# Optimization experiments

Measured on AMD Instinct MI355X. Metric: run time of the kernel, lower is better.

## Reference

```python
import jax, jax.numpy as jnp
import numpy as np

B, F, D = 4096, 64, 256  # batch, feature fields, embedding dim


def setup_inputs() -> dict:
    key = jax.random.key(0)
    inputs = jax.random.normal(key, (B, F, D), dtype=jnp.float32)
    return {"inputs": inputs}


def reference(inputs) -> jnp.ndarray:
    # Batched Gram matrix over the field axis: [B, F, F]
    gram = jnp.einsum('bid,bjd->bij', inputs, inputs)
    # Strict upper triangle (i < j), matching matrix_band_part(0,-1) - band_part(0,0)
    f = inputs.shape[1]
    iu, ju = jnp.triu_indices(f, k=1)
    # Gather the F*(F-1)/2 pairwise interactions per batch row -> [B, P]
    return gram[:, iu, ju]
```

## Files before the change

kernel.cpp:

```cpp
#include <hip/hip_runtime.h>

#define BATCH 4096
#define FF 64
#define DD 256
#define PAD 264
#define NPAIR 2016

typedef __attribute__((ext_vector_type(8))) short short8;
typedef __attribute__((ext_vector_type(16))) float f32x16;

__device__ __forceinline__ unsigned short f2bf(float f) {
    unsigned int u = __float_as_uint(f);
    u += 0x7FFFu + ((u >> 16) & 1u);
    return (unsigned short)(u >> 16);
}

__global__ __launch_bounds__(256, 4) void gram_tri(const float* __restrict__ x,
                                                   float* __restrict__ out) {
    __shared__ __align__(16) unsigned short sX[FF * PAD];
    const int b = blockIdx.x;
    const int t = threadIdx.x;

    const float4* __restrict__ src = (const float4*)(x + (size_t)b * (FF * DD));
#pragma unroll
    for (int it = 0; it < 16; ++it) {
        int idx = (it << 8) + t;
        float4 v = src[idx];
        int r  = idx >> 6;
        int kq = idx & 63;
        ushort4 w;
        w.x = f2bf(v.x); w.y = f2bf(v.y); w.z = f2bf(v.z); w.w = f2bf(v.w);
        *(ushort4*)&sX[r * PAD + (kq << 2)] = w;
    }
    __syncthreads();

    const int wave = t >> 6;
    const int lane = t & 63;
    const int qi = wave >> 1;
    const int qj = wave & 1;
    const int rA = (qi << 5) + (lane & 31);
    const int rB = (qj << 5) + (lane & 31);
    const int ks = (lane >> 5) << 3;

    f32x16 acc;
#pragma unroll
    for (int i = 0; i < 16; ++i) acc[i] = 0.0f;

    const unsigned short* pA = &sX[rA * PAD + ks];
    const unsigned short* pB = &sX[rB * PAD + ks];
#pragma unroll
    for (int ko = 0; ko < DD; ko += 16) {
        short8 a  = *(const short8*)(pA + ko);
        short8 bb = *(const short8*)(pB + ko);
        acc = __builtin_amdgcn_mfma_f32_32x32x16_bf16(a, bb, acc, 0, 0, 0);
    }

    float* __restrict__ ob = out + (size_t)b * NPAIR;
#pragma unroll
    for (int reg = 0; reg < 16; ++reg) {
        int i = (qi << 5) + (reg & 3) + ((reg >> 2) << 3) + ((lane >> 5) << 2);
        int j = (qj << 5) + (lane & 31);
        if (i < j) {
            int p = i * 63 - ((i * (i - 1)) >> 1) + (j - i - 1);
            ob[p] = acc[reg];
        }
    }
}

extern "C" void kernel_launch(void* const* d_in, const int* in_sizes, int n_in,
                              void* d_out, int out_size, void* d_ws, size_t ws_size,
                              hipStream_t stream) {
    const float* x = (const float*)d_in[0];
    float* out = (float*)d_out;
    gram_tri<<<BATCH, 256, 0, stream>>>(x, out);
}
```

Before: 361.2 us.

## Pipeline batch rows through double-buffered LDS chunks and skip lower-quadrant wave

Each block now processes four batch rows in half-K chunks. It prefetches the next chunk into registers while MFMA runs on the current LDS buffer, then writes the converted bf16 data into the alternate buffer. The wave that would compute the lower-left quadrant (entirely i>j) skips its MFMAs and stores, and pairs of floats are packed into bf16 words. This aims to hide global load latency behind compute. In exchange it uses fewer blocks, holds more registers for the prefetch, and adds a barrier per chunk.

```diff
diff --git a/kernel.cpp b/kernel.cpp
--- a/kernel.cpp
+++ b/kernel.cpp
@@ -1,68 +1,107 @@
 #include <hip/hip_runtime.h>
 
-#define BATCH 4096
 #define FF 64
 #define DD 256
-#define PAD 264
+#define KC 128
+#define LSTR 136
 #define NPAIR 2016
+#define ROWS 4
+#define NCHUNK (2 * ROWS)
 
 typedef __attribute__((ext_vector_type(8))) short short8;
 typedef __attribute__((ext_vector_type(16))) float f32x16;
 
-__device__ __forceinline__ unsigned short f2bf(float f) {
-    unsigned int u = __float_as_uint(f);
-    u += 0x7FFFu + ((u >> 16) & 1u);
-    return (unsigned short)(u >> 16);
+__device__ __forceinline__ unsigned int pack2(float lo, float hi) {
+    unsigned int a = __float_as_uint(lo);
+    unsigned int b = __float_as_uint(hi);
+    a += 0x7FFFu + ((a >> 16) & 1u);
+    b += 0x7FFFu + ((b >> 16) & 1u);
+    return (a >> 16) | (b & 0xFFFF0000u);
 }
 
 __global__ __launch_bounds__(256, 4) void gram_tri(const float* __restrict__ x,
                                                    float* __restrict__ out) {
-    __shared__ __align__(16) unsigned short sX[FF * PAD];
-    const int b = blockIdx.x;
+    __shared__ __align__(16) unsigned short sbuf[2][FF * LSTR];
     const int t = threadIdx.x;
+    const int wave = t >> 6;
+    const int lane = t & 63;
+    const int b0 = blockIdx.x * ROWS;
 
-    const float4* __restrict__ src = (const float4*)(x + (size_t)b * (FF * DD));
+    const int qi = wave >> 1, qj = wave & 1;
+    const unsigned short* ldsA0 = &sbuf[0][(qi * 32 + (lane & 31)) * LSTR + ((lane >> 5) << 3)];
+    const unsigned short* ldsB0 = &sbuf[0][(qj * 32 + (lane & 31)) * LSTR + ((lane >> 5) << 3)];
+    const int bufoff = FF * LSTR;
+
+    float4 sr[8];
+    f32x16 acc;
+
+    {
+        const float4* __restrict__ src = (const float4*)(x + (size_t)b0 * (FF * DD));
 #pragma unroll
-    for (int it = 0; it < 16; ++it) {
-        int idx = (it << 8) + t;
-        float4 v = src[idx];
-        int r  = idx >> 6;
-        int kq = idx & 63;
-        ushort4 w;
-        w.x = f2bf(v.x); w.y = f2bf(v.y); w.z = f2bf(v.z); w.w = f2bf(v.w);
-        *(ushort4*)&sX[r * PAD + (kq << 2)] = w;
+        for (int it = 0; it < 8; ++it) {
+            int lin = (it << 8) + t;
+            sr[it] = src[((lin >> 5) << 6) + (lin & 31)];
+        }
+#pragma unroll
+        for (int it = 0; it < 8; ++it) {
+            int lin = (it << 8) + t;
+            int f = lin >> 5, kq = lin & 31;
+            uint2 w;
+            w.x = pack2(sr[it].x, sr[it].y);
+            w.y = pack2(sr[it].z, sr[it].w);
+            *(uint2*)&sbuf[0][f * LSTR + (kq << 2)] = w;
+        }
     }
     __syncthreads();
 
-    const int wave = t >> 6;
-    const int lane = t & 63;
-    const int qi = wave >> 1;
-    const int qj = wave & 1;
-    const int rA = (qi << 5) + (lane & 31);
-    const int rB = (qj << 5) + (lane & 31);
-    const int ks = (lane >> 5) << 3;
-
-    f32x16 acc;
 #pragma unroll
-    for (int i = 0; i < 16; ++i) acc[i] = 0.0f;
-
-    const unsigned short* pA = &sX[rA * PAD + ks];
-    const unsigned short* pB = &sX[rB * PAD + ks];
+    for (int s = 0; s < NCHUNK; ++s) {
+        if (s + 1 < NCHUNK) {
+            int nb = b0 + ((s + 1) >> 1);
+            int kc = ((s + 1) & 1) * KC;
+            const float4* __restrict__ src = (const float4*)(x + (size_t)nb * (FF * DD) + kc);
 #pragma unroll
-    for (int ko = 0; ko < DD; ko += 16) {
-        short8 a  = *(const short8*)(pA + ko);
-        short8 bb = *(const short8*)(pB + ko);
-        acc = __builtin_amdgcn_mfma_f32_32x32x16_bf16(a, bb, acc, 0, 0, 0);
-    }
-
-    float* __restrict__ ob = out + (size_t)b * NPAIR;
+            for (int it = 0; it < 8; ++it) {
+                int lin = (it << 8) + t;
+                sr[it] = src[((lin >> 5) << 6) + (lin & 31)];
+            }
+        }
+        if ((s & 1) == 0) {
 #pragma unroll
-    for (int reg = 0; reg < 16; ++reg) {
-        int i = (qi << 5) + (reg & 3) + ((reg >> 2) << 3) + ((lane >> 5) << 2);
-        int j = (qj << 5) + (lane & 31);
-        if (i < j) {
-            int p = i * 63 - ((i * (i - 1)) >> 1) + (j - i - 1);
-            ob[p] = acc[reg];
+            for (int i = 0; i < 16; ++i) acc[i] = 0.0f;
+        }
+        if (wave != 2) {
+            const unsigned short* pA = ldsA0 + (s & 1) * bufoff;
+            const unsigned short* pB = ldsB0 + (s & 1) * bufoff;
+#pragma unroll
+            for (int ko = 0; ko < KC; ko += 16) {
+                short8 a  = *(const short8*)(pA + ko);
+                short8 bb = *(const short8*)(pB + ko);
+                acc = __builtin_amdgcn_mfma_f32_32x32x16_bf16(a, bb, acc, 0, 0, 0);
+            }
+        }
+        if (s + 1 < NCHUNK) {
+            unsigned short* dst = &sbuf[0][((s + 1) & 1) * bufoff];
+#pragma unroll
+            for (int it = 0; it < 8; ++it) {
+                int lin = (it << 8) + t;
+                int f = lin >> 5, kq = lin & 31;
+                uint2 w;
+                w.x = pack2(sr[it].x, sr[it].y);
+                w.y = pack2(sr[it].z, sr[it].w);
+                *(uint2*)&dst[f * LSTR + (kq << 2)] = w;
+            }
+        }
+        __syncthreads();
+        if ((s & 1) && wave != 2) {
+            int b = b0 + (s >> 1);
+            float* __restrict__ ob = out + (size_t)b * NPAIR;
+#pragma unroll
+            for (int reg = 0; reg < 16; ++reg) {
+                int i = (qi << 5) + (reg & 3) + ((reg >> 2) << 3) + ((lane >> 5) << 2);
+                int j = (qj << 5) + (lane & 31);
+                if (i < j) ob[i * 63 - ((i * (i - 1)) >> 1) + (j - i - 1)] = acc[reg];
+            }
         }
     }
 }
@@ -72,5 +111,5 @@
                               hipStream_t stream) {
     const float* x = (const float*)d_in[0];
     float* out = (float*)d_out;
-    gram_tri<<<BATCH, 256, 0, stream>>>(x, out);
+    gram_tri<<<4096 / ROWS, 256, 0, stream>>>(x, out);
 }
```

Result: no change. 361.0 us (median of 2 runs) (-0.1%).
